# Optimization experiments

Measured on AMD Instinct MI355X. Metric: run time of the kernel, lower is better.

Reference implementation:

```python
import jax, jax.numpy as jnp
from jax import lax
import numpy as np

B = 2048; IMG = 28; K = 3; CIN = 1; HC = 32; LC = 16; WID = 64; HID = 64
LIS = IMG - 3 * (K - 1)           # 22: latent image size
FLAT = LIS * LIS * HC             # 15488
BLK = WID * LC                    # 1024: hypernet block size
T1 = 10.0; T0 = 0.0; NSTEP = 20   # fixed-step RK4 replaces adaptive dopri5
VAR = 0.1                         # p_z0 diagonal covariance


def _conv(x, w, b):  # w: [Cout,Cin,k,k], VALID conv, stride 1
    y = lax.conv_general_dilated(x, w, (1, 1), 'VALID',
                                 dimension_numbers=('NCHW', 'OIHW', 'NCHW'))
    return y + b[None, :, None, None]


def _convT(x, w, b):  # w: [Cin,Cout,k,k] (pytorch ConvTranspose2d layout)
    wf = jnp.flip(w, (2, 3)).transpose(1, 0, 2, 3)  # -> OIHW, spatially flipped
    y = lax.conv_general_dilated(x, wf, (1, 1), [(K - 1, K - 1), (K - 1, K - 1)],
                                 dimension_numbers=('NCHW', 'OIHW', 'NCHW'))
    return y + b[None, :, None, None]


def _forward(x, c0w, c0b, c1w, c1b, c2w, c2b, elw, elb, dlw, dlb,
             t0w, t0b, t1w, t1b, t2w, t2b, h1w, h1b, h2w, h2b, h3w, h3b):
    # ---- encoder (dropout in eval = identity) ----
    h = jnp.tanh(_conv(x, c0w, c0b))
    h = jnp.tanh(_conv(h, c1w, c1b))
    h = jnp.tanh(_conv(h, c2w, c2b))
    z1 = h.reshape(h.shape[0], -1) @ elw + elb          # [B, LC]
    # ---- decoder ----
    d = jnp.tanh(z1 @ dlw + dlb)                         # [B, FLAT]
    d = d.reshape(-1, HC, LIS, LIS)
    d = jnp.tanh(_convT(d, t0w, t0b))
    d = jnp.tanh(_convT(d, t1w, t1b))
    recon = _convT(d, t2w, t2b)                          # [B, CIN, 28, 28]

    # ---- CNF vector field with analytic trace ----
    def hyper(t):
        p = jnp.tanh(jnp.reshape(jnp.asarray(t, jnp.float32), (1, 1)) @ h1w + h1b)
        p = jnp.tanh(p @ h2w + h2b)
        p = (p @ h3w + h3b).reshape(-1)
        W = p[:BLK].reshape(WID, LC)
        U = p[BLK:2 * BLK].reshape(WID, LC) * jax.nn.sigmoid(p[2 * BLK:3 * BLK].reshape(WID, LC))
        Bb = p[3 * BLK:]                                 # [WID]
        return W, Bb, U

    def f(t, z):
        W, Bb, U = hyper(t)
        hh = jnp.tanh(jnp.einsum('bd,wd->wb', z, W) + Bb[:, None])   # [WID, B]
        dz = jnp.einsum('wb,wd->bd', hh, U) / WID                     # [B, LC]
        s = jnp.sum(W * U, axis=1)                                    # [WID]: sum_i W_w[i]U_w[i]
        tr = jnp.mean((1.0 - hh * hh) * s[:, None], axis=0)           # [B] analytic trace
        return dz, -tr[:, None]

    dt = (T0 - T1) / NSTEP

    def step(state, i):
        z, lp = state
        t = T1 + i * dt
        k1z, k1l = f(t, z)
        k2z, k2l = f(t + 0.5 * dt, z + 0.5 * dt * k1z)
        k3z, k3l = f(t + 0.5 * dt, z + 0.5 * dt * k2z)
        k4z, k4l = f(t + dt, z + dt * k3z)
        z = z + dt / 6.0 * (k1z + 2 * k2z + 2 * k3z + k4z)
        lp = lp + dt / 6.0 * (k1l + 2 * k2l + 2 * k3l + k4l)
        return (z, lp), None

    lp1 = jnp.zeros((z1.shape[0], 1), z1.dtype)
    (z0, lp0), _ = lax.scan(step, (z1, lp1), jnp.arange(NSTEP, dtype=jnp.float32))

    # MultivariateNormal(0, 0.1*I) log_prob
    logp = -0.5 * (LC * jnp.log(2 * jnp.pi) + LC * jnp.log(VAR) + jnp.sum(z0 * z0, -1) / VAR)
    x_probs = jnp.mean(logp - lp0[:, 0])
    return recon, x_probs


def setup_inputs() -> dict:
    key = jax.random.key(0)
    ks = jax.random.split(key, 16)
    n = jax.random.normal
    s = jnp.float32(0.05)
    z = jnp.zeros
    OUT3 = 3 * BLK + WID
    return {
        'x': n(ks[0], (B, CIN, IMG, IMG), jnp.float32),
        'c0w': n(ks[1], (HC, CIN, K, K)) * s, 'c0b': z((HC,)),
        'c1w': n(ks[2], (HC, HC, K, K)) * s, 'c1b': z((HC,)),
        'c2w': n(ks[3], (HC, HC, K, K)) * s, 'c2b': z((HC,)),
        'elw': n(ks[4], (FLAT, LC)) * s, 'elb': z((LC,)),
        'dlw': n(ks[5], (LC, FLAT)) * s, 'dlb': z((FLAT,)),
        't0w': n(ks[6], (HC, HC, K, K)) * s, 't0b': z((HC,)),
        't1w': n(ks[7], (HC, HC, K, K)) * s, 't1b': z((HC,)),
        't2w': n(ks[8], (HC, CIN, K, K)) * s, 't2b': z((CIN,)),
        'h1w': n(ks[9], (1, HID)) * s, 'h1b': z((HID,)),
        'h2w': n(ks[10], (HID, HID)) * s, 'h2b': z((HID,)),
        'h3w': n(ks[11], (HID, OUT3)) * s, 'h3b': z((OUT3,)),
    }


def reference(x, c0w, c0b, c1w, c1b, c2w, c2b, elw, elb, dlw, dlb,
              t0w, t0b, t1w, t1b, t2w, t2b, h1w, h1b, h2w, h2b, h3w, h3b):
    return _forward(x, c0w, c0b, c1w, c1b, c2w, c2b, elw, elb, dlw, dlb,
                    t0w, t0b, t1w, t1b, t2w, t2b, h1w, h1b, h2w, h2b, h3w, h3b)
```

## Files before the change

### kernel.cpp

```cpp
#include <hip/hip_runtime.h>
#include <math.h>

#define Bsz 2048

using bf16x8 = __attribute__((ext_vector_type(8))) short;
using f32x4  = __attribute__((ext_vector_type(4))) float;

__device__ __forceinline__ float fast_tanh(float x){
    float e = __expf(2.0f * x);
    return 1.0f - 2.0f / (e + 1.0f);
}
__device__ __forceinline__ float fast_sigmoid(float x){
    return 1.0f / (1.0f + __expf(-x));
}
__device__ __forceinline__ unsigned short f2b(float f){
    union { float f; unsigned u; } v; v.f = f;
    unsigned r = v.u + 0x7FFFu + ((v.u >> 16) & 1u);
    return (unsigned short)(r >> 16);
}
__device__ __forceinline__ float b2f(unsigned short s){
    union { unsigned u; float f; } v; v.u = ((unsigned)s) << 16;
    return v.f;
}

__device__ __forceinline__ float stage_t(int sidx){
    int i  = sidx >> 2, st = sidx & 3;
    float t = 10.0f - 0.5f * (float)i;
    if (st == 1 || st == 2) t -= 0.25f;
    else if (st == 3)       t -= 0.5f;
    return t;
}

__global__ void k_prep(const float* __restrict__ c1w, const float* __restrict__ c2w,
                       const float* __restrict__ t0w, const float* __restrict__ t1w,
                       const float* __restrict__ elw, const float* __restrict__ dlw,
                       unsigned short* __restrict__ wc1, unsigned short* __restrict__ wc2,
                       unsigned short* __restrict__ wt0, unsigned short* __restrict__ wt1,
                       unsigned short* __restrict__ elwT, unsigned short* __restrict__ dlwT,
                       int full){
    int gsz = gridDim.x * 256;
    for (int i = blockIdx.x*256 + threadIdx.x; i < 9216; i += gsz){
        int ci = i & 31, co = (i >> 5) & 31, s = i >> 10;
        wc1[i] = f2b(c1w[(co*32 + ci)*9 + s]);
        wc2[i] = f2b(c2w[(co*32 + ci)*9 + s]);
        wt0[i] = f2b(t0w[(ci*32 + co)*9 + (8 - s)]);
        wt1[i] = f2b(t1w[(ci*32 + co)*9 + (8 - s)]);
    }
    if (!full) return;
    for (int i = blockIdx.x*256 + threadIdx.x; i < 247808; i += gsz){
        int l = i / 15488, f2 = i - l*15488;
        int pos = f2 >> 5, ci = f2 & 31;
        elwT[i] = f2b(elw[(ci*484 + pos)*16 + l]);
    }
    for (int i = blockIdx.x*256 + threadIdx.x; i < 247808; i += gsz){
        int f2 = i >> 4, l = i & 15;
        int pos = f2 >> 5, ci = f2 & 31;
        dlwT[i] = f2b(dlw[l*15488 + ci*484 + pos]);
    }
}

__global__ void __launch_bounds__(256)
k_conv0(const float* __restrict__ x, const float* __restrict__ c0w,
        const float* __restrict__ c0b, unsigned short* __restrict__ A0,
        int cb, int CH){
    int gid = blockIdx.x*256 + threadIdx.x;
    if (gid >= CH*676) return;
    int b = gid / 676, pos = gid - b*676;
    int y = pos / 26, xx = pos - y*26;
    const float* xin = x + (size_t)(cb + b)*784;
    float v[9];
#pragma unroll
    for (int r = 0; r < 3; r++)
#pragma unroll
        for (int s = 0; s < 3; s++)
            v[r*3+s] = xin[(y+r)*28 + xx + s];
    unsigned short* ob = A0 + (size_t)b*21632 + pos*32;
#pragma unroll
    for (int g = 0; g < 8; g++){
        float a0 = c0b[g*4+0], a1 = c0b[g*4+1], a2 = c0b[g*4+2], a3 = c0b[g*4+3];
#pragma unroll
        for (int k = 0; k < 9; k++){
            a0 += v[k] * c0w[(g*4+0)*9 + k];
            a1 += v[k] * c0w[(g*4+1)*9 + k];
            a2 += v[k] * c0w[(g*4+2)*9 + k];
            a3 += v[k] * c0w[(g*4+3)*9 + k];
        }
        ushort4 o;
        o.x = f2b(fast_tanh(a0)); o.y = f2b(fast_tanh(a1));
        o.z = f2b(fast_tanh(a2)); o.w = f2b(fast_tanh(a3));
        *(ushort4*)(ob + g*4) = o;
    }
}

template<int IL, int OL, int OW, int OOFF, int INS, int OUTS>
__global__ void __launch_bounds__(256)
k_convM(const unsigned short* __restrict__ in, const unsigned short* __restrict__ wg,
        const float* __restrict__ bias, unsigned short* __restrict__ out, int CH){
    constexpr int N  = OL * OL;
    constexpr int NT = (N + 15) / 16;
    const int tid = threadIdx.x;
    const int wave = tid >> 6, lane = tid & 63;
    const int q = lane >> 4, nn = lane & 15;
    const int nw = gridDim.x * 4;

    bf16x8 af[2][9];
#pragma unroll
    for (int mt = 0; mt < 2; mt++)
#pragma unroll
        for (int s = 0; s < 9; s++)
            af[mt][s] = *(const bf16x8*)(wg + s*1024 + (mt*16 + nn)*32 + q*8);
    float4 bc0 = *(const float4*)(bias + q*4);
    float4 bc1 = *(const float4*)(bias + 16 + q*4);

    for (int t = blockIdx.x*4 + wave; t < CH*NT; t += nw){
        int img = t / NT, tt = t - img*NT;
        const unsigned short* inb = in + (size_t)img * INS;
        unsigned short* outb = out + (size_t)img * OUTS;
        int pos = tt*16 + nn;
        int pc  = pos < N ? pos : N - 1;
        int oy = pc / OL, ox = pc - oy*OL;
        const unsigned short* ib = inb + (oy*IL + ox)*32 + q*8;
        f32x4 acc0 = {0.f,0.f,0.f,0.f}, acc1 = {0.f,0.f,0.f,0.f};
#pragma unroll
        for (int r = 0; r < 3; r++){
            bf16x8 b0 = *(const bf16x8*)(ib + (r*IL + 0)*32);
            bf16x8 b1 = *(const bf16x8*)(ib + (r*IL + 1)*32);
            bf16x8 b2 = *(const bf16x8*)(ib + (r*IL + 2)*32);
            acc0 = __builtin_amdgcn_mfma_f32_16x16x32_bf16(af[0][r*3+0], b0, acc0, 0,0,0);
            acc1 = __builtin_amdgcn_mfma_f32_16x16x32_bf16(af[1][r*3+0], b0, acc1, 0,0,0);
            acc0 = __builtin_amdgcn_mfma_f32_16x16x32_bf16(af[0][r*3+1], b1, acc0, 0,0,0);
            acc1 = __builtin_amdgcn_mfma_f32_16x16x32_bf16(af[1][r*3+1], b1, acc1, 0,0,0);
            acc0 = __builtin_amdgcn_mfma_f32_16x16x32_bf16(af[0][r*3+2], b2, acc0, 0,0,0);
            acc1 = __builtin_amdgcn_mfma_f32_16x16x32_bf16(af[1][r*3+2], b2, acc1, 0,0,0);
        }
        if (pos < N){
            int opix = oy*OW + ox + OOFF;
            ushort4 o0, o1;
            o0.x = f2b(fast_tanh(acc0[0] + bc0.x)); o0.y = f2b(fast_tanh(acc0[1] + bc0.y));
            o0.z = f2b(fast_tanh(acc0[2] + bc0.z)); o0.w = f2b(fast_tanh(acc0[3] + bc0.w));
            o1.x = f2b(fast_tanh(acc1[0] + bc1.x)); o1.y = f2b(fast_tanh(acc1[1] + bc1.y));
            o1.z = f2b(fast_tanh(acc1[2] + bc1.z)); o1.w = f2b(fast_tanh(acc1[3] + bc1.w));
            *(ushort4*)(outb + opix*32 + q*4)      = o0;
            *(ushort4*)(outb + opix*32 + 16 + q*4) = o1;
        }
    }
}

__global__ void __launch_bounds__(256)
k_encg(const unsigned short* __restrict__ A2, const unsigned short* __restrict__ elwT,
       const float* __restrict__ elb, float* __restrict__ z1, int cb, int CH){
    __shared__ float red[4][64][4];
    int wave = threadIdx.x >> 6, lane = threadIdx.x & 63;
    int q = lane >> 4, nn = lane & 15;
    int imgb = blockIdx.x*16;
    const unsigned short* ap = A2 + (size_t)(imgb + nn)*15488 + wave*3872 + q*8;
    const unsigned short* bp = elwT + (size_t)nn*15488 + wave*3872 + q*8;
    f32x4 acc = {0.f,0.f,0.f,0.f};
#pragma unroll 4
    for (int kk = 0; kk < 121; kk++){
        bf16x8 a = *(const bf16x8*)(ap + kk*32);
        bf16x8 b = *(const bf16x8*)(bp + kk*32);
        acc = __builtin_amdgcn_mfma_f32_16x16x32_bf16(a, b, acc, 0,0,0);
    }
#pragma unroll
    for (int i = 0; i < 4; i++) red[wave][lane][i] = acc[i];
    __syncthreads();
    if (wave == 0){
        float eb = elb[nn];
#pragma unroll
        for (int i = 0; i < 4; i++){
            float s = red[0][lane][i] + red[1][lane][i] + red[2][lane][i] + red[3][lane][i];
            z1[(size_t)(cb + imgb + q*4 + i)*16 + nn] = s + eb;
        }
    }
}

__global__ void __launch_bounds__(256)
k_halo(unsigned short* __restrict__ D0, unsigned short* __restrict__ D1, int CH){
    int gid = blockIdx.x*256 + threadIdx.x;
    uint4 zq = {0,0,0,0};
    if (gid < CH*676){
        int img = gid / 676, px = gid - img*676;
        int y = px / 26, x = px - y*26;
        if (y < 2 || y >= 24 || x < 2 || x >= 24){
            uint4* p = (uint4*)(D0 + (size_t)img*21632 + px*32);
            p[0] = zq; p[1] = zq; p[2] = zq; p[3] = zq;
        }
    } else {
        int g2 = gid - CH*676;
        if (g2 >= CH*784) return;
        int img = g2 / 784, px = g2 - img*784;
        int y = px / 28, x = px - y*28;
        if (y < 2 || y >= 26 || x < 2 || x >= 26){
            uint4* p = (uint4*)(D1 + (size_t)img*25088 + px*32);
            p[0] = zq; p[1] = zq; p[2] = zq; p[3] = zq;
        }
    }
}

__global__ void __launch_bounds__(256)
k_decg(const float* __restrict__ z1, const unsigned short* __restrict__ dlwT,
       const float* __restrict__ dlb, unsigned short* __restrict__ D0,
       int cb, int CH){
    __shared__ float zl[256];
    int tid = threadIdx.x, ib = blockIdx.y;
    zl[tid] = z1[(size_t)(cb + ib*16 + (tid >> 4))*16 + (tid & 15)];
    __syncthreads();
    int ci = tid & 31, po = tid >> 5;
    int pos = blockIdx.x*8 + po;
    if (pos >= 484) return;
    int y = pos / 22, xx = pos - y*22;
    float bias = dlb[ci*484 + pos];
    const unsigned short* w = dlwT + (size_t)(pos*32 + ci)*16;
    bf16x8 w0 = *(const bf16x8*)(w);
    bf16x8 w1 = *(const bf16x8*)(w + 8);
    float wf[16];
#pragma unroll
    for (int j = 0; j < 8; j++){
        wf[j]   = b2f((unsigned short)w0[j]);
        wf[8+j] = b2f((unsigned short)w1[j]);
    }
    int opix = ((y+2)*26 + xx + 2)*32 + ci;
#pragma unroll 1
    for (int i = 0; i < 16; i++){
        float a = bias;
#pragma unroll
        for (int l = 0; l < 16; l++) a += zl[i*16 + l] * wf[l];
        D0[(size_t)(ib*16 + i)*21632 + opix] = f2b(fast_tanh(a));
    }
}

__global__ void __launch_bounds__(256)
k_convT2(const unsigned short* __restrict__ D2, const float* __restrict__ t2w,
         const float* __restrict__ t2b, float* __restrict__ out, int cb, int CH){
    int gid = blockIdx.x*256 + threadIdx.x;
    if (gid >= CH*784) return;
    int b = gid / 784, o = gid - b*784;
    int y = o / 28, xx = o - y*28;
    const unsigned short* db = D2 + (size_t)b*21632;
    float a = t2b[0];
#pragma unroll
    for (int r = 0; r < 3; r++){
        int iy = y + r - 2;
        if ((unsigned)iy >= 26u) continue;
#pragma unroll
        for (int s = 0; s < 3; s++){
            int ix = xx + s - 2;
            if ((unsigned)ix >= 26u) continue;
            const unsigned short* pp = db + (iy*26 + ix)*32;
            int wi = (2-r)*3 + (2-s);
#pragma unroll
            for (int g = 0; g < 4; g++){
                bf16x8 h = *(const bf16x8*)(pp + g*8);
#pragma unroll
                for (int j = 0; j < 8; j++)
                    a += b2f((unsigned short)h[j]) * t2w[(g*8+j)*9 + wi];
            }
        }
    }
    out[(size_t)(cb + b)*784 + o] = a;
}

template<int LOUT, int INW, int OUTW, int OUTOFF>
__device__ __forceinline__ void conv_gemm(const unsigned short* __restrict__ Wg,
                                          const float* __restrict__ bias,
                                          const unsigned short* inL,
                                          unsigned short* outL, int tid){
    constexpr int N  = LOUT * LOUT;
    constexpr int NT = (N + 15) / 16;
    const int lane  = tid & 63;
    const int wave  = tid >> 6;
    const int mtile = wave & 1;
    const int quad  = lane >> 4;
    const int nn    = lane & 15;
    bf16x8 afr[9];
    const unsigned short* wp = Wg + (mtile*16 + nn)*32 + quad*8;
#pragma unroll
    for (int s = 0; s < 9; s++)
        afr[s] = *(const bf16x8*)(wp + s*1024);
    float4 bco = *(const float4*)(bias + mtile*16 + quad*4);
    for (int t = (wave >> 1); t < NT; t += 2){
        int pos = t*16 + nn;
        int pc  = pos < N ? pos : N - 1;
        int y = pc / LOUT, x = pc - y*LOUT;
        const unsigned short* ib = inL + (y*INW + x)*32 + quad*8;
        f32x4 acc = {0.f, 0.f, 0.f, 0.f};
#pragma unroll
        for (int r = 0; r < 3; r++)
#pragma unroll
            for (int s = 0; s < 3; s++)
                acc = __builtin_amdgcn_mfma_f32_16x16x32_bf16(
                        afr[r*3+s], *(const bf16x8*)(ib + (r*INW + s)*32), acc, 0, 0, 0);
        if (pos < N){
            ushort4 o;
            o.x = f2b(fast_tanh(acc[0] + bco.x));
            o.y = f2b(fast_tanh(acc[1] + bco.y));
            o.z = f2b(fast_tanh(acc[2] + bco.z));
            o.w = f2b(fast_tanh(acc[3] + bco.w));
            int opix = y*OUTW + x + OUTOFF;
            *(ushort4*)(outL + opix*32 + mtile*16 + quad*4) = o;
        }
    }
}

__global__ void __launch_bounds__(256)
k_enc_f(const float* __restrict__ x,
        const float* __restrict__ c0w, const float* __restrict__ c0b,
        const unsigned short* __restrict__ wc1, const float* __restrict__ c1b,
        const unsigned short* __restrict__ wc2, const float* __restrict__ c2b,
        const float* __restrict__ elw, const float* __restrict__ elb,
        float* __restrict__ z1){
    __shared__ float X[784];
    __shared__ __align__(16) unsigned short H0[21632];
    __shared__ __align__(16) unsigned short H1[18432];
    __shared__ __align__(16) unsigned short H2[15488];
    __shared__ float red[16*17];
    const int tid = threadIdx.x, b = blockIdx.x;
    for (int i = tid; i < 784; i += 256) X[i] = x[b*784 + i];
    __syncthreads();
    for (int pos = tid; pos < 676; pos += 256){
        int y = pos / 26, xx = pos - y*26;
        float v[9];
#pragma unroll
        for (int r = 0; r < 3; r++)
#pragma unroll
            for (int s = 0; s < 3; s++)
                v[r*3+s] = X[(y+r)*28 + xx + s];
#pragma unroll
        for (int g = 0; g < 8; g++){
            float a0 = c0b[g*4+0], a1 = c0b[g*4+1], a2 = c0b[g*4+2], a3 = c0b[g*4+3];
#pragma unroll
            for (int k = 0; k < 9; k++){
                a0 += v[k] * c0w[(g*4+0)*9 + k];
                a1 += v[k] * c0w[(g*4+1)*9 + k];
                a2 += v[k] * c0w[(g*4+2)*9 + k];
                a3 += v[k] * c0w[(g*4+3)*9 + k];
            }
            ushort4 o;
            o.x = f2b(fast_tanh(a0)); o.y = f2b(fast_tanh(a1));
            o.z = f2b(fast_tanh(a2)); o.w = f2b(fast_tanh(a3));
            *(ushort4*)(H0 + pos*32 + g*4) = o;
        }
    }
    __syncthreads();
    conv_gemm<24, 26, 24, 0>(wc1, c1b, H0, H1, tid);
    __syncthreads();
    conv_gemm<22, 24, 22, 0>(wc2, c2b, H1, H2, tid);
    __syncthreads();
    {
        int fg = tid >> 4, l = tid & 15;
        float a = 0.f;
        for (int ci = 0; ci < 32; ci++)
            for (int pos = fg; pos < 484; pos += 16)
                a += b2f(H2[pos*32 + ci]) * elw[(ci*484 + pos)*16 + l];
        red[fg*17 + l] = a;
        __syncthreads();
        if (tid < 16){
            float s = elb[tid];
#pragma unroll
            for (int g = 0; g < 16; g++) s += red[g*17 + tid];
            z1[b*16 + tid] = s;
        }
    }
}

__global__ void __launch_bounds__(256)
k_dec_f(const float* __restrict__ z1,
        const float* __restrict__ dlw, const float* __restrict__ dlb,
        const unsigned short* __restrict__ wt0, const float* __restrict__ t0b,
        const unsigned short* __restrict__ wt1, const float* __restrict__ t1b,
        const float* __restrict__ t2w, const float* __restrict__ t2b,
        float* __restrict__ out){
    __shared__ __align__(16) unsigned short D0[21632];
    __shared__ __align__(16) unsigned short D1[25088];
    __shared__ __align__(16) unsigned short D2[28800];
    const int tid = threadIdx.x, b = blockIdx.x;
    {
        uint4 zq = {0,0,0,0};
        for (int i = tid; i < 2704; i += 256) ((uint4*)D0)[i] = zq;
        for (int i = tid; i < 3136; i += 256) ((uint4*)D1)[i] = zq;
        for (int i = tid; i < 3600; i += 256) ((uint4*)D2)[i] = zq;
    }
    float zz[16];
#pragma unroll
    for (int l = 0; l < 16; l++) zz[l] = z1[b*16 + l];
    __syncthreads();
    for (int f = tid; f < 15488; f += 256){
        float a = dlb[f];
#pragma unroll
        for (int l = 0; l < 16; l++) a += zz[l] * dlw[l*15488 + f];
        int ci = f / 484, pos = f - ci*484;
        int y = pos / 22, xx = pos - y*22;
        D0[((y+2)*26 + xx + 2)*32 + ci] = f2b(fast_tanh(a));
    }
    __syncthreads();
    conv_gemm<24, 26, 28, 58>(wt0, t0b, D0, D1, tid);
    __syncthreads();
    conv_gemm<26, 28, 30, 62>(wt1, t1b, D1, D2, tid);
    __syncthreads();
    for (int o = tid; o < 784; o += 256){
        int y = o / 28, xx = o - y*28;
        float a = t2b[0];
#pragma unroll
        for (int r = 0; r < 3; r++)
#pragma unroll
            for (int s = 0; s < 3; s++){
                const unsigned short* pp = D2 + ((y+r)*30 + xx + s)*32;
                int wi = (2-r)*3 + (2-s);
#pragma unroll
                for (int g = 0; g < 4; g++){
                    bf16x8 h = *(const bf16x8*)(pp + g*8);
#pragma unroll
                    for (int j = 0; j < 8; j++)
                        a += b2f((unsigned short)h[j]) * t2w[(g*8+j)*9 + wi];
                }
            }
        out[(size_t)b*784 + o] = a;
    }
}

__global__ void __launch_bounds__(64)
k_hyp1(const float* __restrict__ h1w, const float* __restrict__ h1b,
       const float* __restrict__ h2w, const float* __restrict__ h2b,
       float* __restrict__ p2ws){
    __shared__ float p1l[64];
    int sidx = blockIdx.x, tid = threadIdx.x;
    float t = stage_t(sidx);
    p1l[tid] = fast_tanh(t * h1w[tid] + h1b[tid]);
    __syncthreads();
    float a0 = h2b[tid], a1 = 0.f, a2 = 0.f, a3 = 0.f;
#pragma unroll
    for (int k = 0; k < 64; k += 4){
        a0 += p1l[k]   * h2w[(k)*64   + tid];
        a1 += p1l[k+1] * h2w[(k+1)*64 + tid];
        a2 += p1l[k+2] * h2w[(k+2)*64 + tid];
        a3 += p1l[k+3] * h2w[(k+3)*64 + tid];
    }
    p2ws[sidx*64 + tid] = fast_tanh((a0 + a1) + (a2 + a3));
}

__global__ void __launch_bounds__(256)
k_hyp2(const float* __restrict__ p2ws, const float* __restrict__ h3w,
       const float* __restrict__ h3b, float* __restrict__ p3ws){
    __shared__ float p2l[64];
    int sidx = blockIdx.y, tid = threadIdx.x;
    if (tid < 64) p2l[tid] = p2ws[sidx*64 + tid];
    __syncthreads();
    int m = blockIdx.x*256 + tid;
    if (m >= 3136) return;
    const float* hp = h3w + m;
    float a0 = h3b[m], a1 = 0.f, a2 = 0.f, a3 = 0.f;
#pragma unroll
    for (int k = 0; k < 64; k += 4){
        a0 += p2l[k]   * hp[(size_t)(k)*3136];
        a1 += p2l[k+1] * hp[(size_t)(k+1)*3136];
        a2 += p2l[k+2] * hp[(size_t)(k+2)*3136];
        a3 += p2l[k+3] * hp[(size_t)(k+3)*3136];
    }
    p3ws[(size_t)sidx*3200 + m] = (a0 + a1) + (a2 + a3);
}

__global__ void __launch_bounds__(256)
k_hyp3(const float* __restrict__ p3ws, float* __restrict__ hyp){
    __shared__ float partial[256];
    int sidx = blockIdx.x, tid = threadIdx.x;
    const float* p3 = p3ws + (size_t)sidx*3200;
    float* g = hyp + (size_t)sidx*2304;
    int m0 = tid*4;
    float4 w4 = *(const float4*)(p3 + m0);
    float4 a4 = *(const float4*)(p3 + 1024 + m0);
    float4 s4 = *(const float4*)(p3 + 2048 + m0);
    float4 u4;
    u4.x = a4.x * fast_sigmoid(s4.x);
    u4.y = a4.y * fast_sigmoid(s4.y);
    u4.z = a4.z * fast_sigmoid(s4.z);
    u4.w = a4.w * fast_sigmoid(s4.w);
    *(float4*)(g + m0) = w4;
    g[1024 + ((m0+0) & 15)*64 + ((m0+0) >> 4)] = u4.x;
    g[1024 + ((m0+1) & 15)*64 + ((m0+1) >> 4)] = u4.y;
    g[1024 + ((m0+2) & 15)*64 + ((m0+2) >> 4)] = u4.z;
    g[1024 + ((m0+3) & 15)*64 + ((m0+3) >> 4)] = u4.w;
    partial[tid] = w4.x*u4.x + w4.y*u4.y + w4.z*u4.z + w4.w*u4.w;
    __syncthreads();
    if (tid < 64){
        g[2048 + tid] = p3[3072 + tid];
        g[2112 + tid] = partial[tid*4] + partial[tid*4+1]
                      + partial[tid*4+2] + partial[tid*4+3];
    }
}

__global__ void k_hyper(const float* __restrict__ h1w, const float* __restrict__ h1b,
                        const float* __restrict__ h2w, const float* __restrict__ h2b,
                        const float* __restrict__ h3w, const float* __restrict__ h3b,
                        float* __restrict__ hyp){
    int sidx = blockIdx.x;
    float t = stage_t(sidx);
    __shared__ float p1[64], p2[64];
    __shared__ float p3[3136];
    int tid = threadIdx.x;
    if (tid < 64) p1[tid] = fast_tanh(t * h1w[tid] + h1b[tid]);
    __syncthreads();
    if (tid < 64){
        float a = h2b[tid];
#pragma unroll
        for (int k = 0; k < 64; k++) a += p1[k] * h2w[k*64 + tid];
        p2[tid] = fast_tanh(a);
    }
    __syncthreads();
    for (int m = tid; m < 3136; m += 256){
        float a = h3b[m];
#pragma unroll
        for (int k = 0; k < 64; k++) a += p2[k] * h3w[k*3136 + m];
        p3[m] = a;
    }
    __syncthreads();
    float* g = hyp + (size_t)sidx * 2304;
    for (int m = tid; m < 1024; m += 256){
        g[m] = p3[m];
        float u = p3[1024 + m] * fast_sigmoid(p3[2048 + m]);
        g[1024 + (m & 15)*64 + (m >> 4)] = u;
        p3[1024 + m] = u;
    }
    if (tid < 64) g[2048 + tid] = p3[3072 + tid];
    __syncthreads();
    if (tid < 64){
        float s = 0.f;
#pragma unroll
        for (int d = 0; d < 16; d++) s += p3[tid*16 + d] * p3[1024 + tid*16 + d];
        g[2112 + tid] = s;
    }
}

struct PF { float4 Wr[4]; float4 Ur[4]; float Bb, st; };

__device__ __forceinline__ void load_pf(const float* __restrict__ g, int lane, PF& p){
    const float4* w4 = (const float4*)(g + lane*16);
    p.Wr[0] = w4[0]; p.Wr[1] = w4[1]; p.Wr[2] = w4[2]; p.Wr[3] = w4[3];
    const float4* u4 = (const float4*)(g + 1024 + lane*16);
    p.Ur[0] = u4[0]; p.Ur[1] = u4[1]; p.Ur[2] = u4[2]; p.Ur[3] = u4[3];
    p.Bb = g[2048 + lane];
    p.st = g[2112 + lane];
}

__global__ void __launch_bounds__(64)
k_cnf(const float* __restrict__ z1, const float* __restrict__ hyp,
      float* __restrict__ part){
    __shared__ __align__(16) float Utl[16*68];
    __shared__ __align__(16) float hhl[4*68];
    __shared__ __align__(16) float zsl[64];
    __shared__ __align__(16) float sl[64];
    __shared__ float red2[4];

    const int lane = threadIdx.x;
    const int bloc = lane >> 4, d = lane & 15;
    const int du = lane >> 2, wb = (lane & 3) * 16;
    const float dt = -0.5f;

    float z  = z1[(size_t)(blockIdx.x*4 + bloc)*16 + d];
    float zs = z;
    float lp = 0.f;
    float zacc = 0.f, lacc = 0.f;

    PF cur, nxt;
    load_pf(hyp, lane, cur);

    for (int sidx = 0; sidx < 80; sidx++){
        *(float4*)(Utl + du*68 + wb)      = cur.Ur[0];
        *(float4*)(Utl + du*68 + wb + 4)  = cur.Ur[1];
        *(float4*)(Utl + du*68 + wb + 8)  = cur.Ur[2];
        *(float4*)(Utl + du*68 + wb + 12) = cur.Ur[3];
        sl[lane]  = cur.st;
        zsl[lane] = zs;
        __syncthreads();
        if (sidx < 79) load_pf(hyp + (size_t)(sidx + 1)*2304, lane, nxt);

        float hhv[4];
#pragma unroll
        for (int b = 0; b < 4; b++){
            const float4* zp = (const float4*)(zsl + b*16);
            float4 z0 = zp[0], z1v = zp[1], z2 = zp[2], z3 = zp[3];
            float a = cur.Bb;
            a += z0.x*cur.Wr[0].x + z0.y*cur.Wr[0].y + z0.z*cur.Wr[0].z + z0.w*cur.Wr[0].w;
            a += z1v.x*cur.Wr[1].x + z1v.y*cur.Wr[1].y + z1v.z*cur.Wr[1].z + z1v.w*cur.Wr[1].w;
            a += z2.x*cur.Wr[2].x + z2.y*cur.Wr[2].y + z2.z*cur.Wr[2].z + z2.w*cur.Wr[2].w;
            a += z3.x*cur.Wr[3].x + z3.y*cur.Wr[3].y + z3.z*cur.Wr[3].z + z3.w*cur.Wr[3].w;
            hhv[b] = fast_tanh(a);
        }
#pragma unroll
        for (int b = 0; b < 4; b++) hhl[b*68 + lane] = hhv[b];
        __syncthreads();

        float dz = 0.f;
        const float4* h4p = (const float4*)(hhl + bloc*68);
        const float4* u4p = (const float4*)(Utl + d*68);
#pragma unroll
        for (int w4 = 0; w4 < 16; w4++){
            float4 h = h4p[w4], u = u4p[w4];
            dz += h.x*u.x + h.y*u.y + h.z*u.z + h.w*u.w;
        }
        float4 hh4 = h4p[d];
        float4 s4  = ((const float4*)sl)[d];
        float tr = (1.f - hh4.x*hh4.x)*s4.x + (1.f - hh4.y*hh4.y)*s4.y
                 + (1.f - hh4.z*hh4.z)*s4.z + (1.f - hh4.w*hh4.w)*s4.w;
#pragma unroll
        for (int off = 1; off < 16; off <<= 1)
            tr += __shfl_xor(tr, off, 16);
        dz *= (1.f/64.f);
        float dl = -tr * (1.f/64.f);

        int st = sidx & 3;
        float wgt = (st == 0 || st == 3) ? 1.f : 2.f;
        zacc += wgt * dz;
        lacc += wgt * dl;
        if (st < 3){
            float a = (st == 2) ? 1.0f : 0.5f;
            zs = z + a * dt * dz;
        } else {
            z  += (dt/6.f) * zacc;
            lp += (dt/6.f) * lacc;
            zs = z;
            zacc = 0.f; lacc = 0.f;
        }
        cur = nxt;
    }

    float sq = z * z;
#pragma unroll
    for (int off = 1; off < 16; off <<= 1) sq += __shfl_xor(sq, off, 16);
    float logp = -0.5f * (16.f*1.8378770664093453f + 16.f*(-2.302585092994046f) + sq*10.f);
    float contrib = logp - lp;
    if (d == 0) red2[bloc] = contrib;
    __syncthreads();
    if (lane == 0)
        part[blockIdx.x] = red2[0] + red2[1] + red2[2] + red2[3];
}

__global__ void k_final(const float* __restrict__ part, float* __restrict__ out){
    __shared__ float red[256];
    int tid = threadIdx.x;
    red[tid] = part[tid] + part[tid + 256];
    __syncthreads();
    for (int s = 128; s > 0; s >>= 1){
        if (tid < s) red[tid] += red[tid + s];
        __syncthreads();
    }
    if (tid == 0) out[1605632] = red[0] * (1.f/2048.f);
}

extern "C" void kernel_launch(void* const* d_in, const int* in_sizes, int n_in,
                              void* d_out, int out_size, void* d_ws, size_t ws_size,
                              hipStream_t stream){
    const float* x   = (const float*)d_in[0];
    const float* c0w = (const float*)d_in[1];
    const float* c0b = (const float*)d_in[2];
    const float* c1w = (const float*)d_in[3];
    const float* c1b = (const float*)d_in[4];
    const float* c2w = (const float*)d_in[5];
    const float* c2b = (const float*)d_in[6];
    const float* elw = (const float*)d_in[7];
    const float* elb = (const float*)d_in[8];
    const float* dlw = (const float*)d_in[9];
    const float* dlb = (const float*)d_in[10];
    const float* t0w = (const float*)d_in[11];
    const float* t0b = (const float*)d_in[12];
    const float* t1w = (const float*)d_in[13];
    const float* t1b = (const float*)d_in[14];
    const float* t2w = (const float*)d_in[15];
    const float* t2b = (const float*)d_in[16];
    const float* h1w = (const float*)d_in[17];
    const float* h1b = (const float*)d_in[18];
    const float* h2w = (const float*)d_in[19];
    const float* h2b = (const float*)d_in[20];
    const float* h3w = (const float*)d_in[21];
    const float* h3b = (const float*)d_in[22];

    float* ws   = (float*)d_ws;
    float* z1   = ws;
    float* hyp  = z1 + 32768;
    float* part = hyp + 184320;
    float* p2ws = part + 512;
    float* p3ws = p2ws + 5120;
    unsigned short* wc1  = (unsigned short*)(p3ws + 256000);
    unsigned short* wc2  = wc1 + 9216;
    unsigned short* wt0  = wc2 + 9216;
    unsigned short* wt1  = wt0 + 9216;
    unsigned short* elwT = wt1 + 9216;
    unsigned short* dlwT = elwT + 247808;
    unsigned short* act  = dlwT + 247808;
    float* rec  = (float*)d_out;

    const size_t MISC = 2979840;
    int CH = 0;
    const int cands[6] = {2048, 1024, 512, 256, 128, 64};
    for (int c = 0; c < 6; c++){
        size_t need = MISC + (size_t)cands[c] * 111104;
        if (need <= ws_size){ CH = cands[c]; break; }
    }

    if (CH == 0){
        k_hyper<<<80, 256, 0, stream>>>(h1w, h1b, h2w, h2b, h3w, h3b, hyp);
        k_prep <<<64,   256, 0, stream>>>(c1w, c2w, t0w, t1w, elw, dlw,
                                          wc1, wc2, wt0, wt1, wt1, wt1, 0);
        k_enc_f<<<2048, 256, 0, stream>>>(x, c0w, c0b, wc1, c1b, wc2, c2b, elw, elb, z1);
        k_cnf  <<<512,   64, 0, stream>>>(z1, hyp, part);
        k_dec_f<<<2048, 256, 0, stream>>>(z1, dlw, dlb, wt0, t0b, wt1, t1b, t2w, t2b, rec);
        k_final<<<1,    256, 0, stream>>>(part, rec);
        return;
    }

    k_hyp1<<<80,           64, 0, stream>>>(h1w, h1b, h2w, h2b, p2ws);
    k_hyp2<<<dim3(13,80), 256, 0, stream>>>(p2ws, h3w, h3b, p3ws);
    k_hyp3<<<80,          256, 0, stream>>>(p3ws, hyp);

    k_prep<<<64, 256, 0, stream>>>(c1w, c2w, t0w, t1w, elw, dlw,
                                   wc1, wc2, wt0, wt1, elwT, dlwT, 1);

    unsigned short* R0 = act;
    unsigned short* R1 = R0 + (size_t)CH*21632;
    unsigned short* R2 = R1 + (size_t)CH*18432;
    unsigned short* D1 = R1;

    for (int cb = 0; cb < Bsz; cb += CH){
        k_conv0<<<(CH*676 + 255)/256, 256, 0, stream>>>(x, c0w, c0b, R0, cb, CH);
        k_convM<26,24,24, 0, 21632, 18432><<<(CH*36 + 15)/16, 256, 0, stream>>>(R0, wc1, c1b, R1, CH);
        k_convM<24,22,22, 0, 18432, 15488><<<(CH*31 + 15)/16, 256, 0, stream>>>(R1, wc2, c2b, R2, CH);
        k_encg<<<CH/16, 256, 0, stream>>>(R2, elwT, elb, z1, cb, CH);
        k_halo<<<(CH*1460 + 255)/256, 256, 0, stream>>>(R0, D1, CH);
        k_decg<<<dim3(61, CH/16), 256, 0, stream>>>(z1, dlwT, dlb, R0, cb, CH);
        k_convM<26,24,28,58, 21632, 25088><<<(CH*36 + 15)/16, 256, 0, stream>>>(R0, wt0, t0b, D1, CH);
        k_convM<28,26,26, 0, 25088, 21632><<<(CH*43 + 15)/16, 256, 0, stream>>>(D1, wt1, t1b, R0, CH);
        k_convT2<<<(CH*784 + 255)/256, 256, 0, stream>>>(R0, t2w, t2b, rec, cb, CH);
    }
    k_cnf  <<<512,  64, 0, stream>>>(z1, hyp, part);
    k_final<<<1,   256, 0, stream>>>(part, rec);
}
```

Baseline: 666.2 us.

## Split encoder GEMV over K with atomics; one sample per CNF block

The encoder linear kernel now splits its K dimension across four grid slices and accumulates with float atomics into z1, which k_prep pre-initializes with the bias. This removes the shared-memory reduction and raises the block count. The CNF kernel is restructured so each 64-thread block integrates one sample instead of four. Trace and dz are computed through wave shuffles rather than shared-memory tiles, and the grid grows to 2048 blocks. This adds atomic contention and makes summation order nondeterministic. Each block also reloads the hypernet weights, since they are no longer shared across four samples.

```diff
diff --git a/kernel.cpp b/kernel.cpp
--- a/kernel.cpp
+++ b/kernel.cpp
@@ -34,10 +34,11 @@
 __global__ void k_prep(const float* __restrict__ c1w, const float* __restrict__ c2w,
                        const float* __restrict__ t0w, const float* __restrict__ t1w,
                        const float* __restrict__ elw, const float* __restrict__ dlw,
+                       const float* __restrict__ elb,
                        unsigned short* __restrict__ wc1, unsigned short* __restrict__ wc2,
                        unsigned short* __restrict__ wt0, unsigned short* __restrict__ wt1,
                        unsigned short* __restrict__ elwT, unsigned short* __restrict__ dlwT,
-                       int full){
+                       float* __restrict__ z1, int full){
     int gsz = gridDim.x * 256;
     for (int i = blockIdx.x*256 + threadIdx.x; i < 9216; i += gsz){
         int ci = i & 31, co = (i >> 5) & 31, s = i >> 10;
@@ -47,6 +48,8 @@
         wt1[i] = f2b(t1w[(ci*32 + co)*9 + (8 - s)]);
     }
     if (!full) return;
+    for (int i = blockIdx.x*256 + threadIdx.x; i < 32768; i += gsz)
+        z1[i] = elb[i & 15];
     for (int i = blockIdx.x*256 + threadIdx.x; i < 247808; i += gsz){
         int l = i / 15488, f2 = i - l*15488;
         int pos = f2 >> 5, ci = f2 & 31;
@@ -148,31 +151,24 @@
 
 __global__ void __launch_bounds__(256)
 k_encg(const unsigned short* __restrict__ A2, const unsigned short* __restrict__ elwT,
-       const float* __restrict__ elb, float* __restrict__ z1, int cb, int CH){
-    __shared__ float red[4][64][4];
+       float* __restrict__ z1, int cb, int CH){
     int wave = threadIdx.x >> 6, lane = threadIdx.x & 63;
     int q = lane >> 4, nn = lane & 15;
     int imgb = blockIdx.x*16;
-    const unsigned short* ap = A2 + (size_t)(imgb + nn)*15488 + wave*3872 + q*8;
-    const unsigned short* bp = elwT + (size_t)nn*15488 + wave*3872 + q*8;
+    const unsigned short* ap = A2 + (size_t)(imgb + nn)*15488 + q*8;
+    const unsigned short* bp = elwT + (size_t)nn*15488 + q*8;
     f32x4 acc = {0.f,0.f,0.f,0.f};
-#pragma unroll 4
-    for (int kk = 0; kk < 121; kk++){
-        bf16x8 a = *(const bf16x8*)(ap + kk*32);
-        bf16x8 b = *(const bf16x8*)(bp + kk*32);
+    int s0 = blockIdx.y*121;
+#pragma unroll 2
+    for (int s = s0 + wave; s < s0 + 121; s += 4){
+        bf16x8 a = *(const bf16x8*)(ap + s*32);
+        bf16x8 b = *(const bf16x8*)(bp + s*32);
         acc = __builtin_amdgcn_mfma_f32_16x16x32_bf16(a, b, acc, 0,0,0);
     }
-#pragma unroll
-    for (int i = 0; i < 4; i++) red[wave][lane][i] = acc[i];
-    __syncthreads();
-    if (wave == 0){
-        float eb = elb[nn];
-#pragma unroll
-        for (int i = 0; i < 4; i++){
-            float s = red[0][lane][i] + red[1][lane][i] + red[2][lane][i] + red[3][lane][i];
-            z1[(size_t)(cb + imgb + q*4 + i)*16 + nn] = s + eb;
-        }
-    }
+    float* zp = z1 + (size_t)(cb + imgb)*16;
+#pragma unroll
+    for (int i = 0; i < 4; i++)
+        atomicAdd(zp + (q*4 + i)*16 + nn, acc[i]);
 }
 
 __global__ void __launch_bounds__(256)
@@ -531,96 +527,80 @@
     }
 }
 
-struct PF { float4 Wr[4]; float4 Ur[4]; float Bb, st; };
-
-__device__ __forceinline__ void load_pf(const float* __restrict__ g, int lane, PF& p){
+struct PF { float4 Wr[4]; float4 Ur[4]; float Bb, sw; };
+
+__device__ __forceinline__ void load_pf(const float* __restrict__ g,
+                                        int lane, int q, int d, PF& p){
     const float4* w4 = (const float4*)(g + lane*16);
     p.Wr[0] = w4[0]; p.Wr[1] = w4[1]; p.Wr[2] = w4[2]; p.Wr[3] = w4[3];
-    const float4* u4 = (const float4*)(g + 1024 + lane*16);
+    const float4* u4 = (const float4*)(g + 1024 + d*64 + q*16);
     p.Ur[0] = u4[0]; p.Ur[1] = u4[1]; p.Ur[2] = u4[2]; p.Ur[3] = u4[3];
     p.Bb = g[2048 + lane];
-    p.st = g[2112 + lane];
+    p.sw = g[2112 + lane];
 }
 
 __global__ void __launch_bounds__(64)
 k_cnf(const float* __restrict__ z1, const float* __restrict__ hyp,
       float* __restrict__ part){
-    __shared__ __align__(16) float Utl[16*68];
-    __shared__ __align__(16) float hhl[4*68];
-    __shared__ __align__(16) float zsl[64];
-    __shared__ __align__(16) float sl[64];
-    __shared__ float red2[4];
-
+    __shared__ __align__(16) float zsl[16];
+    __shared__ __align__(16) float hhl[64];
     const int lane = threadIdx.x;
-    const int bloc = lane >> 4, d = lane & 15;
-    const int du = lane >> 2, wb = (lane & 3) * 16;
+    const int q = lane >> 4, d = lane & 15;
     const float dt = -0.5f;
 
-    float z  = z1[(size_t)(blockIdx.x*4 + bloc)*16 + d];
+    float z  = z1[(size_t)blockIdx.x*16 + d];
     float zs = z;
-    float lp = 0.f;
-    float zacc = 0.f, lacc = 0.f;
+    float lp = 0.f, zacc = 0.f, lacc = 0.f;
+    if (lane < 16) zsl[lane] = zs;
 
     PF cur, nxt;
-    load_pf(hyp, lane, cur);
+    load_pf(hyp, lane, q, d, cur);
 
     for (int sidx = 0; sidx < 80; sidx++){
-        *(float4*)(Utl + du*68 + wb)      = cur.Ur[0];
-        *(float4*)(Utl + du*68 + wb + 4)  = cur.Ur[1];
-        *(float4*)(Utl + du*68 + wb + 8)  = cur.Ur[2];
-        *(float4*)(Utl + du*68 + wb + 12) = cur.Ur[3];
-        sl[lane]  = cur.st;
-        zsl[lane] = zs;
         __syncthreads();
-        if (sidx < 79) load_pf(hyp + (size_t)(sidx + 1)*2304, lane, nxt);
-
-        float hhv[4];
-#pragma unroll
-        for (int b = 0; b < 4; b++){
-            const float4* zp = (const float4*)(zsl + b*16);
-            float4 z0 = zp[0], z1v = zp[1], z2 = zp[2], z3 = zp[3];
-            float a = cur.Bb;
-            a += z0.x*cur.Wr[0].x + z0.y*cur.Wr[0].y + z0.z*cur.Wr[0].z + z0.w*cur.Wr[0].w;
-            a += z1v.x*cur.Wr[1].x + z1v.y*cur.Wr[1].y + z1v.z*cur.Wr[1].z + z1v.w*cur.Wr[1].w;
-            a += z2.x*cur.Wr[2].x + z2.y*cur.Wr[2].y + z2.z*cur.Wr[2].z + z2.w*cur.Wr[2].w;
-            a += z3.x*cur.Wr[3].x + z3.y*cur.Wr[3].y + z3.z*cur.Wr[3].z + z3.w*cur.Wr[3].w;
-            hhv[b] = fast_tanh(a);
-        }
-#pragma unroll
-        for (int b = 0; b < 4; b++) hhl[b*68 + lane] = hhv[b];
+        if (sidx < 79) load_pf(hyp + (size_t)(sidx + 1)*2304, lane, q, d, nxt);
+
+        const float4* zp = (const float4*)zsl;
+        float4 z0 = zp[0], z1v = zp[1], z2 = zp[2], z3 = zp[3];
+        float a = cur.Bb;
+        a += z0.x*cur.Wr[0].x + z0.y*cur.Wr[0].y + z0.z*cur.Wr[0].z + z0.w*cur.Wr[0].w;
+        a += z1v.x*cur.Wr[1].x + z1v.y*cur.Wr[1].y + z1v.z*cur.Wr[1].z + z1v.w*cur.Wr[1].w;
+        a += z2.x*cur.Wr[2].x + z2.y*cur.Wr[2].y + z2.z*cur.Wr[2].z + z2.w*cur.Wr[2].w;
+        a += z3.x*cur.Wr[3].x + z3.y*cur.Wr[3].y + z3.z*cur.Wr[3].z + z3.w*cur.Wr[3].w;
+        float hh = fast_tanh(a);
+        float e = (1.f - hh*hh) * cur.sw;
+#pragma unroll
+        for (int off = 1; off < 64; off <<= 1)
+            e += __shfl_xor(e, off);
+        hhl[lane] = hh;
         __syncthreads();
 
-        float dz = 0.f;
-        const float4* h4p = (const float4*)(hhl + bloc*68);
-        const float4* u4p = (const float4*)(Utl + d*68);
-#pragma unroll
-        for (int w4 = 0; w4 < 16; w4++){
-            float4 h = h4p[w4], u = u4p[w4];
-            dz += h.x*u.x + h.y*u.y + h.z*u.z + h.w*u.w;
-        }
-        float4 hh4 = h4p[d];
-        float4 s4  = ((const float4*)sl)[d];
-        float tr = (1.f - hh4.x*hh4.x)*s4.x + (1.f - hh4.y*hh4.y)*s4.y
-                 + (1.f - hh4.z*hh4.z)*s4.z + (1.f - hh4.w*hh4.w)*s4.w;
-#pragma unroll
-        for (int off = 1; off < 16; off <<= 1)
-            tr += __shfl_xor(tr, off, 16);
-        dz *= (1.f/64.f);
-        float dl = -tr * (1.f/64.f);
+        const float4* hp = (const float4*)(hhl + q*16);
+        float4 h0 = hp[0], h1 = hp[1], h2 = hp[2], h3 = hp[3];
+        float dzp = 0.f;
+        dzp += h0.x*cur.Ur[0].x + h0.y*cur.Ur[0].y + h0.z*cur.Ur[0].z + h0.w*cur.Ur[0].w;
+        dzp += h1.x*cur.Ur[1].x + h1.y*cur.Ur[1].y + h1.z*cur.Ur[1].z + h1.w*cur.Ur[1].w;
+        dzp += h2.x*cur.Ur[2].x + h2.y*cur.Ur[2].y + h2.z*cur.Ur[2].z + h2.w*cur.Ur[2].w;
+        dzp += h3.x*cur.Ur[3].x + h3.y*cur.Ur[3].y + h3.z*cur.Ur[3].z + h3.w*cur.Ur[3].w;
+        dzp += __shfl_xor(dzp, 16);
+        dzp += __shfl_xor(dzp, 32);
+        float dz = dzp * (1.f/64.f);
+        float dl = -e  * (1.f/64.f);
 
         int st = sidx & 3;
         float wgt = (st == 0 || st == 3) ? 1.f : 2.f;
         zacc += wgt * dz;
         lacc += wgt * dl;
         if (st < 3){
-            float a = (st == 2) ? 1.0f : 0.5f;
-            zs = z + a * dt * dz;
+            float aa = (st == 2) ? 1.0f : 0.5f;
+            zs = z + aa * dt * dz;
         } else {
             z  += (dt/6.f) * zacc;
             lp += (dt/6.f) * lacc;
             zs = z;
             zacc = 0.f; lacc = 0.f;
         }
+        if (lane < 16) zsl[lane] = zs;
         cur = nxt;
     }
 
@@ -628,20 +608,19 @@
 #pragma unroll
     for (int off = 1; off < 16; off <<= 1) sq += __shfl_xor(sq, off, 16);
     float logp = -0.5f * (16.f*1.8378770664093453f + 16.f*(-2.302585092994046f) + sq*10.f);
-    float contrib = logp - lp;
-    if (d == 0) red2[bloc] = contrib;
-    __syncthreads();
-    if (lane == 0)
-        part[blockIdx.x] = red2[0] + red2[1] + red2[2] + red2[3];
+    if (lane == 0) part[blockIdx.x] = logp - lp;
 }
 
 __global__ void k_final(const float* __restrict__ part, float* __restrict__ out){
     __shared__ float red[256];
     int tid = threadIdx.x;
-    red[tid] = part[tid] + part[tid + 256];
-    __syncthreads();
-    for (int s = 128; s > 0; s >>= 1){
-        if (tid < s) red[tid] += red[tid + s];
+    float s = 0.f;
+#pragma unroll
+    for (int k = 0; k < 8; k++) s += part[tid + k*256];
+    red[tid] = s;
+    __syncthreads();
+    for (int st = 128; st > 0; st >>= 1){
+        if (tid < st) red[tid] += red[tid + st];
         __syncthreads();
     }
     if (tid == 0) out[1605632] = red[0] * (1.f/2048.f);
@@ -678,7 +657,7 @@
     float* z1   = ws;
     float* hyp  = z1 + 32768;
     float* part = hyp + 184320;
-    float* p2ws = part + 512;
+    float* p2ws = part + 2048;
     float* p3ws = p2ws + 5120;
     unsigned short* wc1  = (unsigned short*)(p3ws + 256000);
     unsigned short* wc2  = wc1 + 9216;
@@ -689,7 +668,7 @@
     unsigned short* act  = dlwT + 247808;
     float* rec  = (float*)d_out;
 
-    const size_t MISC = 2979840;
+    const size_t MISC = 2985984;
     int CH = 0;
     const int cands[6] = {2048, 1024, 512, 256, 128, 64};
     for (int c = 0; c < 6; c++){
@@ -699,10 +678,10 @@
 
     if (CH == 0){
         k_hyper<<<80, 256, 0, stream>>>(h1w, h1b, h2w, h2b, h3w, h3b, hyp);
-        k_prep <<<64,   256, 0, stream>>>(c1w, c2w, t0w, t1w, elw, dlw,
-                                          wc1, wc2, wt0, wt1, wt1, wt1, 0);
+        k_prep <<<64,   256, 0, stream>>>(c1w, c2w, t0w, t1w, elw, dlw, elb,
+                                          wc1, wc2, wt0, wt1, wt1, wt1, z1, 0);
         k_enc_f<<<2048, 256, 0, stream>>>(x, c0w, c0b, wc1, c1b, wc2, c2b, elw, elb, z1);
-        k_cnf  <<<512,   64, 0, stream>>>(z1, hyp, part);
+        k_cnf  <<<2048,  64, 0, stream>>>(z1, hyp, part);
         k_dec_f<<<2048, 256, 0, stream>>>(z1, dlw, dlb, wt0, t0b, wt1, t1b, t2w, t2b, rec);
         k_final<<<1,    256, 0, stream>>>(part, rec);
         return;
@@ -712,8 +691,8 @@
     k_hyp2<<<dim3(13,80), 256, 0, stream>>>(p2ws, h3w, h3b, p3ws);
     k_hyp3<<<80,          256, 0, stream>>>(p3ws, hyp);
 
-    k_prep<<<64, 256, 0, stream>>>(c1w, c2w, t0w, t1w, elw, dlw,
-                                   wc1, wc2, wt0, wt1, elwT, dlwT, 1);
+    k_prep<<<64, 256, 0, stream>>>(c1w, c2w, t0w, t1w, elw, dlw, elb,
+                                   wc1, wc2, wt0, wt1, elwT, dlwT, z1, 1);
 
     unsigned short* R0 = act;
     unsigned short* R1 = R0 + (size_t)CH*21632;
@@ -724,13 +703,13 @@
         k_conv0<<<(CH*676 + 255)/256, 256, 0, stream>>>(x, c0w, c0b, R0, cb, CH);
         k_convM<26,24,24, 0, 21632, 18432><<<(CH*36 + 15)/16, 256, 0, stream>>>(R0, wc1, c1b, R1, CH);
         k_convM<24,22,22, 0, 18432, 15488><<<(CH*31 + 15)/16, 256, 0, stream>>>(R1, wc2, c2b, R2, CH);
-        k_encg<<<CH/16, 256, 0, stream>>>(R2, elwT, elb, z1, cb, CH);
+        k_encg<<<dim3(CH/16, 4), 256, 0, stream>>>(R2, elwT, z1, cb, CH);
         k_halo<<<(CH*1460 + 255)/256, 256, 0, stream>>>(R0, D1, CH);
         k_decg<<<dim3(61, CH/16), 256, 0, stream>>>(z1, dlwT, dlb, R0, cb, CH);
         k_convM<26,24,28,58, 21632, 25088><<<(CH*36 + 15)/16, 256, 0, stream>>>(R0, wt0, t0b, D1, CH);
         k_convM<28,26,26, 0, 25088, 21632><<<(CH*43 + 15)/16, 256, 0, stream>>>(D1, wt1, t1b, R0, CH);
         k_convT2<<<(CH*784 + 255)/256, 256, 0, stream>>>(R0, t2w, t2b, rec, cb, CH);
     }
-    k_cnf  <<<512,  64, 0, stream>>>(z1, hyp, part);
-    k_final<<<1,   256, 0, stream>>>(part, rec);
-}
+    k_cnf  <<<2048,  64, 0, stream>>>(z1, hyp, part);
+    k_final<<<1,    256, 0, stream>>>(part, rec);
+}
```

After: 662.6 us. About the same (-0.5%).
